# Kernel tuning notes

Measured on AMD Instinct MI355X. Metric: run time of the kernel, lower is better.

The kernel has to match this reference:

```python
import jax, jax.numpy as jnp
import numpy as np

N = 100000     # graph nodes (users + items)
NNZ = 3200000  # edges, avg degree 32
D = 128        # latent_dim
H = 64         # latent_dim // 2


def setup_inputs() -> dict:
    key = jax.random.key(0)
    ks = jax.random.split(key, 6)
    x = jax.random.normal(ks[0], (N, D), jnp.float32)
    rows = jax.random.randint(ks[1], (NNZ,), 0, N, jnp.int32)
    cols = jax.random.randint(ks[2], (NNZ,), 0, N, jnp.int32)
    # positive values ~ normalized adjacency weights
    vals = jax.random.uniform(ks[3], (NNZ,), jnp.float32) / 32.0
    # torch Linear convention: weight [out, in], xavier-uniform init, bias 0.01
    W1 = jax.random.normal(ks[4], (H, D), jnp.float32) * (6.0 / (D + H)) ** 0.5
    b1 = jnp.full((H,), 0.01, jnp.float32)
    W2 = jax.random.normal(ks[5], (1, H), jnp.float32) * (6.0 / (H + 1)) ** 0.5
    b2 = jnp.full((1,), 0.01, jnp.float32)
    t = jnp.zeros((1,), jnp.float32)  # ODE time, unused by the math
    return dict(t=t, x=x, rows=rows, cols=cols, vals=vals, W1=W1, b1=b1, W2=W2, b2=b2)


def _spmm(rows, cols, vals, x):
    # sparse (COO) @ dense: out[r] += vals[e] * x[cols[e]] for edges e with rows[e]==r
    return jax.ops.segment_sum(vals[:, None] * x[cols], rows, num_segments=x.shape[0])


def reference(t, x, rows, cols, vals, W1, b1, W2, b2):
    # gate: sigmoid(Linear(clamp(Linear(x))))  -> [N, 1]
    hidden = jnp.clip(x @ W1.T + b1, -10.0, 10.0)
    alph = jax.nn.sigmoid(hidden @ W2.T + b2)
    alph = jnp.clip(alph, 1e-6, 1.0 - 1e-6)
    # two-hop graph diffusion: alph * (A @ (A @ x)) - x
    ax = _spmm(rows, cols, vals, x)
    ax = alph * _spmm(rows, cols, vals, ax)
    return ax - x
```

## Files before the change

### kernel.cpp

```cpp
#include <hip/hip_runtime.h>
#include <stdint.h>

typedef unsigned int uint;
typedef unsigned short ushort;
typedef float f32x2 __attribute__((ext_vector_type(2)));
typedef float f32x4v __attribute__((ext_vector_type(4)));
typedef short short8 __attribute__((ext_vector_type(8)));

#define NBC_MAX 512
#define VAL7_SCALE 4064.0f
#define VAL7_INV   (1.0f / 4064.0f)
#define CUR_STRIDE 16

__device__ __forceinline__ ushort f2bf(float f) {
    uint u = __float_as_uint(f);
    return (ushort)((u + 0x7fffu + ((u >> 16) & 1u)) >> 16);
}


__global__ __launch_bounds__(256) void k_bhist(const int* __restrict__ rows,
                                               uint* __restrict__ bhist, int nnz, int nb) {
    __shared__ uint h[NBC_MAX];
    for (int j = threadIdx.x; j < nb; j += blockDim.x) h[j] = 0;
    __syncthreads();
    int stride = gridDim.x * blockDim.x;
    for (int i = blockIdx.x * blockDim.x + threadIdx.x; i < nnz; i += stride)
        atomicAdd(&h[rows[i] >> 8], 1u);
    __syncthreads();
    for (int j = threadIdx.x; j < nb; j += blockDim.x) {
        uint c = h[j];
        if (c) atomicAdd(&bhist[j], c);
    }
}


__global__ __launch_bounds__(256) void k_scan(const uint* __restrict__ bhist,
                                              uint* __restrict__ off, uint* __restrict__ cur,
                                              uint* __restrict__ row_off,
                                              int nb, int nnz, int N) {
    __shared__ uint wsum[4];
    __shared__ uint carry;
    int t = threadIdx.x, lane = t & 63, wv = t >> 6;
    if (t == 0) carry = 0;
    __syncthreads();
    for (int base = 0; base < nb; base += 256) {
        int i = base + t;
        uint v = (i < nb) ? bhist[i] : 0u;
        uint inc = v;
#pragma unroll
        for (int o = 1; o < 64; o <<= 1) { uint u = __shfl_up(inc, o); if (lane >= o) inc += u; }
        if (lane == 63) wsum[wv] = inc;
        __syncthreads();
        uint woff = 0;
        for (int k = 0; k < wv; k++) woff += wsum[k];
        uint excl = carry + woff + (inc - v);
        if (i < nb) { off[i] = excl; cur[i * CUR_STRIDE] = excl; }
        uint tot = wsum[0] + wsum[1] + wsum[2] + wsum[3];
        __syncthreads();
        if (t == 0) carry += tot;
        __syncthreads();
    }
    if (t == 0) { off[nb] = (uint)nnz; row_off[N] = (uint)nnz; }
}


__global__ __launch_bounds__(512) void k_binpass(const int* __restrict__ rows,
                                                 const int* __restrict__ cols,
                                                 const float* __restrict__ vals,
                                                 uint* __restrict__ cur, uint* __restrict__ stage,
                                                 int nnz, int nb) {
    __shared__ uint lh[NBC_MAX];
    __shared__ uint gb[NBC_MAX];
    long long beg = ((long long)blockIdx.x * nnz) / gridDim.x;
    long long end = ((long long)(blockIdx.x + 1) * nnz) / gridDim.x;
    for (int j = threadIdx.x; j < nb; j += blockDim.x) lh[j] = 0;
    __syncthreads();
    {
        long long i = beg + threadIdx.x;
        for (; i + 1536 < end; i += 2048) {
            int r0 = __builtin_nontemporal_load(rows + i);
            int r1 = __builtin_nontemporal_load(rows + i + 512);
            int r2 = __builtin_nontemporal_load(rows + i + 1024);
            int r3 = __builtin_nontemporal_load(rows + i + 1536);
            atomicAdd(&lh[r0 >> 8], 1u);
            atomicAdd(&lh[r1 >> 8], 1u);
            atomicAdd(&lh[r2 >> 8], 1u);
            atomicAdd(&lh[r3 >> 8], 1u);
        }
        for (; i < end; i += 512)
            atomicAdd(&lh[__builtin_nontemporal_load(rows + i) >> 8], 1u);
    }
    __syncthreads();
    for (int j = threadIdx.x; j < nb; j += blockDim.x) {
        uint c = lh[j];
        gb[j] = c ? atomicAdd(&cur[j * CUR_STRIDE], c) : 0u;
        lh[j] = 0;
    }
    __syncthreads();
    {
        long long i = beg + threadIdx.x;
        for (; i + 1536 < end; i += 2048) {
            int r0 = __builtin_nontemporal_load(rows + i);
            int r1 = __builtin_nontemporal_load(rows + i + 512);
            int r2 = __builtin_nontemporal_load(rows + i + 1024);
            int r3 = __builtin_nontemporal_load(rows + i + 1536);
            uint c0 = (uint)__builtin_nontemporal_load(cols + i);
            uint c1 = (uint)__builtin_nontemporal_load(cols + i + 512);
            uint c2 = (uint)__builtin_nontemporal_load(cols + i + 1024);
            uint c3 = (uint)__builtin_nontemporal_load(cols + i + 1536);
            float v0 = __builtin_nontemporal_load(vals + i);
            float v1 = __builtin_nontemporal_load(vals + i + 512);
            float v2 = __builtin_nontemporal_load(vals + i + 1024);
            float v3 = __builtin_nontemporal_load(vals + i + 1536);
            uint p0 = gb[r0 >> 8] + atomicAdd(&lh[r0 >> 8], 1u);
            uint p1 = gb[r1 >> 8] + atomicAdd(&lh[r1 >> 8], 1u);
            uint p2 = gb[r2 >> 8] + atomicAdd(&lh[r2 >> 8], 1u);
            uint p3 = gb[r3 >> 8] + atomicAdd(&lh[r3 >> 8], 1u);
            uint q0 = (uint)fminf(v0 * VAL7_SCALE + 0.5f, 127.f);
            uint q1 = (uint)fminf(v1 * VAL7_SCALE + 0.5f, 127.f);
            uint q2 = (uint)fminf(v2 * VAL7_SCALE + 0.5f, 127.f);
            uint q3 = (uint)fminf(v3 * VAL7_SCALE + 0.5f, 127.f);
            stage[p0] = ((uint)(r0 & 255) << 24) | (c0 << 7) | q0;
            stage[p1] = ((uint)(r1 & 255) << 24) | (c1 << 7) | q1;
            stage[p2] = ((uint)(r2 & 255) << 24) | (c2 << 7) | q2;
            stage[p3] = ((uint)(r3 & 255) << 24) | (c3 << 7) | q3;
        }
        for (; i < end; i += 512) {
            int r = __builtin_nontemporal_load(rows + i);
            int b = r >> 8;
            uint pos = gb[b] + atomicAdd(&lh[b], 1u);
            uint c = (uint)__builtin_nontemporal_load(cols + i);
            float v = __builtin_nontemporal_load(vals + i);
            uint q = (uint)fminf(v * VAL7_SCALE + 0.5f, 127.f);
            stage[pos] = ((uint)(r & 255) << 24) | (c << 7) | q;
        }
    }
}


__global__ __launch_bounds__(1024) void k_bsort(const uint* __restrict__ boff,
                                                const uint* __restrict__ stage,
                                                uint* __restrict__ sorted,
                                                uint* __restrict__ row_off,
                                                int N) {
    __shared__ uint rcnt[256], rcur[256];
    __shared__ uint wsum[4];
    int b = blockIdx.x;
    uint s = boff[b], e = boff[b + 1];
    int t = threadIdx.x;
    if (t < 256) rcnt[t] = 0;
    __syncthreads();
    for (uint i = s + t; i < e; i += blockDim.x)
        atomicAdd(&rcnt[stage[i] >> 24], 1u);
    __syncthreads();
    int lane = t & 63, wv = t >> 6;
    uint v = 0, inc = 0;
    if (t < 256) {
        v = rcnt[t];
        inc = v;
#pragma unroll
        for (int o = 1; o < 64; o <<= 1) { uint u = __shfl_up(inc, o); if (lane >= o) inc += u; }
        if (lane == 63) wsum[wv] = inc;
    }
    __syncthreads();
    if (t < 256) {
        uint woff = 0;
        for (int k = 0; k < wv; k++) woff += wsum[k];
        uint excl = woff + inc - v;
        rcur[t] = excl;
        int r = (b << 8) + t;
        if (r < N) row_off[r] = s + excl;
    }
    __syncthreads();
    for (uint i = s + t; i < e; i += blockDim.x) {
        uint rec = stage[i];
        uint pos = atomicAdd(&rcur[rec >> 24], 1u);
        sorted[s + pos] = rec & 0x00FFFFFFu;
    }
}


__global__ __launch_bounds__(256) void k_gatemfma(const float* __restrict__ x,
                                                  const float* __restrict__ W1,
                                                  const float* __restrict__ b1,
                                                  const float* __restrict__ W2,
                                                  const float* __restrict__ b2,
                                                  float* __restrict__ alph,
                                                  unsigned char* __restrict__ xf8, int N) {
    int lane = threadIdx.x & 63;
    int gw = (blockIdx.x * blockDim.x + threadIdx.x) >> 6;
    int nwaves = (gridDim.x * blockDim.x) >> 6;
    int g = lane >> 4;
    int r16 = lane & 15;

    short8 Bfrag[4][4];
#pragma unroll
    for (int c = 0; c < 4; c++) {
        const float* wrow = W1 + (size_t)(c * 16 + r16) * 128 + g * 8;
#pragma unroll
        for (int t = 0; t < 4; t++) {
            float4 f0 = *(const float4*)(wrow + t * 32);
            float4 f1 = *(const float4*)(wrow + t * 32 + 4);
            short8 s;
            s[0] = (short)f2bf(f0.x); s[1] = (short)f2bf(f0.y);
            s[2] = (short)f2bf(f0.z); s[3] = (short)f2bf(f0.w);
            s[4] = (short)f2bf(f1.x); s[5] = (short)f2bf(f1.y);
            s[6] = (short)f2bf(f1.z); s[7] = (short)f2bf(f1.w);
            Bfrag[c][t] = s;
        }
    }
    float b1c[4], w2c[4];
#pragma unroll
    for (int c = 0; c < 4; c++) { b1c[c] = b1[c * 16 + r16]; w2c[c] = W2[c * 16 + r16]; }
    float b2s = b2[0];

    int ntiles = (N + 15) >> 4;
    for (int tile = gw; tile < ntiles; tile += nwaves) {
        int n0 = tile << 4;
        int nrow = n0 + r16;
        int nclamp = nrow < N ? nrow : N - 1;
        const float* xrow = x + ((size_t)nclamp << 7) + g * 8;
        f32x4v acc0 = {0.f, 0.f, 0.f, 0.f}, acc1 = {0.f, 0.f, 0.f, 0.f};
        f32x4v acc2 = {0.f, 0.f, 0.f, 0.f}, acc3 = {0.f, 0.f, 0.f, 0.f};
#pragma unroll
        for (int t = 0; t < 4; t++) {
            float4 f0 = *(const float4*)(xrow + t * 32);
            float4 f1 = *(const float4*)(xrow + t * 32 + 4);
            if (nrow < N) {
                int pk0 = __builtin_amdgcn_cvt_pk_fp8_f32(f0.x, f0.y, 0, false);
                pk0 = __builtin_amdgcn_cvt_pk_fp8_f32(f0.z, f0.w, pk0, true);
                int pk1 = __builtin_amdgcn_cvt_pk_fp8_f32(f1.x, f1.y, 0, false);
                pk1 = __builtin_amdgcn_cvt_pk_fp8_f32(f1.z, f1.w, pk1, true);
                uint* xb = (uint*)(xf8 + ((size_t)nrow << 7) + t * 32 + g * 8);
                xb[0] = (uint)pk0;
                xb[1] = (uint)pk1;
            }
            short8 A;
            A[0] = (short)f2bf(f0.x); A[1] = (short)f2bf(f0.y);
            A[2] = (short)f2bf(f0.z); A[3] = (short)f2bf(f0.w);
            A[4] = (short)f2bf(f1.x); A[5] = (short)f2bf(f1.y);
            A[6] = (short)f2bf(f1.z); A[7] = (short)f2bf(f1.w);
            acc0 = __builtin_amdgcn_mfma_f32_16x16x32_bf16(A, Bfrag[0][t], acc0, 0, 0, 0);
            acc1 = __builtin_amdgcn_mfma_f32_16x16x32_bf16(A, Bfrag[1][t], acc1, 0, 0, 0);
            acc2 = __builtin_amdgcn_mfma_f32_16x16x32_bf16(A, Bfrag[2][t], acc2, 0, 0, 0);
            acc3 = __builtin_amdgcn_mfma_f32_16x16x32_bf16(A, Bfrag[3][t], acc3, 0, 0, 0);
        }
        float pr0 = 0.f, pr1 = 0.f, pr2 = 0.f, pr3 = 0.f;
#pragma unroll
        for (int r = 0; r < 4; r++) {
            float h0 = fminf(fmaxf(acc0[r] + b1c[0], -10.f), 10.f) * w2c[0];
            float h1 = fminf(fmaxf(acc1[r] + b1c[1], -10.f), 10.f) * w2c[1];
            float h2 = fminf(fmaxf(acc2[r] + b1c[2], -10.f), 10.f) * w2c[2];
            float h3 = fminf(fmaxf(acc3[r] + b1c[3], -10.f), 10.f) * w2c[3];
            float s = (h0 + h1) + (h2 + h3);
            if (r == 0) pr0 = s; else if (r == 1) pr1 = s;
            else if (r == 2) pr2 = s; else pr3 = s;
        }
#pragma unroll
        for (int o = 1; o < 16; o <<= 1) {
            pr0 += __shfl_xor(pr0, o);
            pr1 += __shfl_xor(pr1, o);
            pr2 += __shfl_xor(pr2, o);
            pr3 += __shfl_xor(pr3, o);
        }
        if (r16 < 4) {
            float p = r16 == 0 ? pr0 : r16 == 1 ? pr1 : r16 == 2 ? pr2 : pr3;
            float a = 1.f / (1.f + __expf(-(p + b2s)));
            a = fminf(fmaxf(a, 1e-6f), 1.f - 1e-6f);
            int node = n0 + g * 4 + r16;
            if (node < N) alph[node] = a;
        }
    }
}


__global__ __launch_bounds__(256) void k_spmm1(const uint* __restrict__ roff,
                                               const uint* __restrict__ recs,
                                               const unsigned char* __restrict__ xf8,
                                               unsigned char* __restrict__ axf8, int N) {
    int w = (blockIdx.x * blockDim.x + threadIdx.x) >> 6;
    int lane = threadIdx.x & 63;
    if (w >= N) return;
    uint beg = (uint)__builtin_amdgcn_readfirstlane(roff[w]);
    uint end = (uint)__builtin_amdgcn_readfirstlane(roff[w + 1]);
    float s0[8], s1[8];
#pragma unroll
    for (int k = 0; k < 8; k++) { s0[k] = 0.f; s1[k] = 0.f; }
    uint e = beg;
    for (; e + 8 <= end; e += 8) {
#pragma unroll
        for (int k = 0; k < 8; k++) {
            uint q = __builtin_nontemporal_load(recs + e + k);
            ushort u = *(const ushort*)(xf8 + ((size_t)(q >> 7) << 7) + (lane << 1));
            float v = (float)(q & 0x7Fu) * VAL7_INV;
            f32x2 f = __builtin_amdgcn_cvt_pk_f32_fp8((int)u, false);
            s0[k] = fmaf(v, f.x, s0[k]);
            s1[k] = fmaf(v, f.y, s1[k]);
        }
    }
    for (; e < end; e++) {
        uint q = __builtin_nontemporal_load(recs + e);
        ushort u = *(const ushort*)(xf8 + ((size_t)(q >> 7) << 7) + (lane << 1));
        float v = (float)(q & 0x7Fu) * VAL7_INV;
        f32x2 f = __builtin_amdgcn_cvt_pk_f32_fp8((int)u, false);
        s0[0] = fmaf(v, f.x, s0[0]);
        s1[0] = fmaf(v, f.y, s1[0]);
    }
    float a0 = ((s0[0] + s0[1]) + (s0[2] + s0[3])) + ((s0[4] + s0[5]) + (s0[6] + s0[7]));
    float a1 = ((s1[0] + s1[1]) + (s1[2] + s1[3])) + ((s1[4] + s1[5]) + (s1[6] + s1[7]));
    int pk = __builtin_amdgcn_cvt_pk_fp8_f32(a0, a1, 0, false);
    *(ushort*)(axf8 + ((size_t)w << 7) + (lane << 1)) = (ushort)(pk & 0xffff);
}


__global__ __launch_bounds__(256) void k_spmm2(const uint* __restrict__ roff,
                                               const uint* __restrict__ recs,
                                               const unsigned char* __restrict__ axf8,
                                               const float* __restrict__ alph,
                                               const float* __restrict__ x,
                                               float* __restrict__ out, int N) {
    int w = (blockIdx.x * blockDim.x + threadIdx.x) >> 6;
    int lane = threadIdx.x & 63;
    if (w >= N) return;
    uint beg = (uint)__builtin_amdgcn_readfirstlane(roff[w]);
    uint end = (uint)__builtin_amdgcn_readfirstlane(roff[w + 1]);
    float s0[8], s1[8];
#pragma unroll
    for (int k = 0; k < 8; k++) { s0[k] = 0.f; s1[k] = 0.f; }
    uint e = beg;
    for (; e + 8 <= end; e += 8) {
#pragma unroll
        for (int k = 0; k < 8; k++) {
            uint q = __builtin_nontemporal_load(recs + e + k);
            ushort u = *(const ushort*)(axf8 + ((size_t)(q >> 7) << 7) + (lane << 1));
            float v = (float)(q & 0x7Fu) * VAL7_INV;
            f32x2 f = __builtin_amdgcn_cvt_pk_f32_fp8((int)u, false);
            s0[k] = fmaf(v, f.x, s0[k]);
            s1[k] = fmaf(v, f.y, s1[k]);
        }
    }
    for (; e < end; e++) {
        uint q = __builtin_nontemporal_load(recs + e);
        ushort u = *(const ushort*)(axf8 + ((size_t)(q >> 7) << 7) + (lane << 1));
        float v = (float)(q & 0x7Fu) * VAL7_INV;
        f32x2 f = __builtin_amdgcn_cvt_pk_f32_fp8((int)u, false);
        s0[0] = fmaf(v, f.x, s0[0]);
        s1[0] = fmaf(v, f.y, s1[0]);
    }
    float a0 = ((s0[0] + s0[1]) + (s0[2] + s0[3])) + ((s0[4] + s0[5]) + (s0[6] + s0[7]));
    float a1 = ((s1[0] + s1[1]) + (s1[2] + s1[3])) + ((s1[4] + s1[5]) + (s1[6] + s1[7]));
    float al = alph[w];
    const f32x2* xp = (const f32x2*)(x + ((size_t)w << 7)) + lane;
    f32x2 xr = __builtin_nontemporal_load(xp);
    f32x2 o;
    o.x = fmaf(al, a0, -xr.x);
    o.y = fmaf(al, a1, -xr.y);
    __builtin_nontemporal_store(o, (f32x2*)out + ((size_t)w << 6) + lane);
}


extern "C" void kernel_launch(void* const* d_in, const int* in_sizes, int n_in,
                              void* d_out, int out_size, void* d_ws, size_t ws_size,
                              hipStream_t stream) {
    const float* x    = (const float*)d_in[1];
    const int*   rows = (const int*)d_in[2];
    const int*   cols = (const int*)d_in[3];
    const float* vals = (const float*)d_in[4];
    const float* W1 = (const float*)d_in[5];
    const float* b1 = (const float*)d_in[6];
    const float* W2 = (const float*)d_in[7];
    const float* b2 = (const float*)d_in[8];
    float* out = (float*)d_out;

    int N = in_sizes[1] / 128;
    int nnz = in_sizes[2];
    int nb = (N + 255) >> 8;

    char* ws = (char*)d_ws;
    size_t off_b = 0;
    auto take = [&](size_t bytes) -> char* {
        size_t p = (off_b + 255) & ~(size_t)255;
        off_b = p + bytes;
        return ws + p;
    };
    uint*   stage  = (uint*)take((size_t)nnz * 4);
    unsigned char* xf8 = (unsigned char*)take((size_t)N * 128);
    uint*   sorted = (uint*)take((size_t)nnz * 4);
    unsigned char* axf8 = (unsigned char*)take((size_t)N * 128);
    float*  alph   = (float*)take((size_t)N * 4);
    uint*   bhist  = (uint*)take((size_t)(nb + 1) * 4);
    uint*   boff   = (uint*)take((size_t)(nb + 1) * 4);
    uint*   bcur   = (uint*)take((size_t)(nb + 1) * 4 * CUR_STRIDE);
    uint*   row_off = (uint*)take((size_t)(N + 1) * 4);
    (void)ws_size; (void)n_in; (void)out_size;

    hipMemsetAsync(bhist, 0, (size_t)nb * 4, stream);
    k_bhist<<<120, 256, 0, stream>>>(rows, bhist, nnz, nb);
    k_scan<<<1, 256, 0, stream>>>(bhist, boff, bcur, row_off, nb, nnz, N);
    k_binpass<<<1024, 512, 0, stream>>>(rows, cols, vals, bcur, stage, nnz, nb);
    k_bsort<<<nb, 1024, 0, stream>>>(boff, stage, sorted, row_off, N);
    k_gatemfma<<<512, 256, 0, stream>>>(x, W1, b1, W2, b2, alph, xf8, N);
    k_spmm1<<<((N * 64) + 255) / 256, 256, 0, stream>>>(row_off, sorted, xf8, axf8, N);
    k_spmm2<<<((N * 64) + 255) / 256, 256, 0, stream>>>(row_off, sorted, axf8, alph, x, out, N);
}
```

Measured before the change: 296.6 us.

## Replace atomic bin cursor with per-block count matrix and two-level scan

The bucket sort pre-pass previously built a global histogram, scanned it, then had each binning block reserve space with global atomics on bin cursors, reading the rows array three times. It now writes per-block bin counts to a matrix, scans each bin column across blocks, and scans the bin totals, so the scatter kernel gets deterministic offsets without global atomics. This removes the separate histogram pass and the cursor contention, at the cost of a 1024×nb count matrix and two extra small kernel launches. The k_cscan kernel hardcodes 16 counts per lane across 64 lanes, which ties it to NBLK=1024.

New measurement: 251.7 us. -15.1%, faster.

```diff
diff --git a/kernel.cpp b/kernel.cpp
--- a/kernel.cpp
+++ b/kernel.cpp
@@ -8,9 +8,9 @@
 typedef short short8 __attribute__((ext_vector_type(8)));
 
 #define NBC_MAX 512
+#define NBLK 1024
 #define VAL7_SCALE 4064.0f
 #define VAL7_INV   (1.0f / 4064.0f)
-#define CUR_STRIDE 16
 
 __device__ __forceinline__ ushort f2bf(float f) {
     uint u = __float_as_uint(f);
@@ -18,59 +18,9 @@
 }
 
 
-__global__ __launch_bounds__(256) void k_bhist(const int* __restrict__ rows,
-                                               uint* __restrict__ bhist, int nnz, int nb) {
-    __shared__ uint h[NBC_MAX];
-    for (int j = threadIdx.x; j < nb; j += blockDim.x) h[j] = 0;
-    __syncthreads();
-    int stride = gridDim.x * blockDim.x;
-    for (int i = blockIdx.x * blockDim.x + threadIdx.x; i < nnz; i += stride)
-        atomicAdd(&h[rows[i] >> 8], 1u);
-    __syncthreads();
-    for (int j = threadIdx.x; j < nb; j += blockDim.x) {
-        uint c = h[j];
-        if (c) atomicAdd(&bhist[j], c);
-    }
-}
-
-
-__global__ __launch_bounds__(256) void k_scan(const uint* __restrict__ bhist,
-                                              uint* __restrict__ off, uint* __restrict__ cur,
-                                              uint* __restrict__ row_off,
-                                              int nb, int nnz, int N) {
-    __shared__ uint wsum[4];
-    __shared__ uint carry;
-    int t = threadIdx.x, lane = t & 63, wv = t >> 6;
-    if (t == 0) carry = 0;
-    __syncthreads();
-    for (int base = 0; base < nb; base += 256) {
-        int i = base + t;
-        uint v = (i < nb) ? bhist[i] : 0u;
-        uint inc = v;
-#pragma unroll
-        for (int o = 1; o < 64; o <<= 1) { uint u = __shfl_up(inc, o); if (lane >= o) inc += u; }
-        if (lane == 63) wsum[wv] = inc;
-        __syncthreads();
-        uint woff = 0;
-        for (int k = 0; k < wv; k++) woff += wsum[k];
-        uint excl = carry + woff + (inc - v);
-        if (i < nb) { off[i] = excl; cur[i * CUR_STRIDE] = excl; }
-        uint tot = wsum[0] + wsum[1] + wsum[2] + wsum[3];
-        __syncthreads();
-        if (t == 0) carry += tot;
-        __syncthreads();
-    }
-    if (t == 0) { off[nb] = (uint)nnz; row_off[N] = (uint)nnz; }
-}
-
-
-__global__ __launch_bounds__(512) void k_binpass(const int* __restrict__ rows,
-                                                 const int* __restrict__ cols,
-                                                 const float* __restrict__ vals,
-                                                 uint* __restrict__ cur, uint* __restrict__ stage,
-                                                 int nnz, int nb) {
+__global__ __launch_bounds__(512) void k_count(const int* __restrict__ rows,
+                                               uint* __restrict__ C, int nnz, int nb) {
     __shared__ uint lh[NBC_MAX];
-    __shared__ uint gb[NBC_MAX];
     long long beg = ((long long)blockIdx.x * nnz) / gridDim.x;
     long long end = ((long long)(blockIdx.x + 1) * nnz) / gridDim.x;
     for (int j = threadIdx.x; j < nb; j += blockDim.x) lh[j] = 0;
@@ -91,10 +41,81 @@
             atomicAdd(&lh[__builtin_nontemporal_load(rows + i) >> 8], 1u);
     }
     __syncthreads();
+    for (int j = threadIdx.x; j < nb; j += blockDim.x)
+        C[(size_t)blockIdx.x * nb + j] = lh[j];
+}
+
+
+__global__ __launch_bounds__(256) void k_cscan(uint* __restrict__ C,
+                                               uint* __restrict__ T, int nb) {
+    int wv = (blockIdx.x * blockDim.x + threadIdx.x) >> 6;
+    int lane = threadIdx.x & 63;
+    if (wv >= nb) return;
+    uint v[16];
+    uint s = 0;
+#pragma unroll
+    for (int k = 0; k < 16; k++) {
+        v[k] = C[(size_t)(lane * 16 + k) * nb + wv];
+        s += v[k];
+    }
+    uint inc = s;
+#pragma unroll
+    for (int o = 1; o < 64; o <<= 1) { uint u = __shfl_up(inc, o); if (lane >= o) inc += u; }
+    uint run = inc - s;
+#pragma unroll
+    for (int k = 0; k < 16; k++) {
+        uint t = v[k];
+        C[(size_t)(lane * 16 + k) * nb + wv] = run;
+        run += t;
+    }
+    if (lane == 63) T[wv] = inc;
+}
+
+
+__global__ __launch_bounds__(256) void k_scan(const uint* __restrict__ T,
+                                              uint* __restrict__ off,
+                                              uint* __restrict__ row_off,
+                                              int nb, int nnz, int N) {
+    __shared__ uint wsum[4];
+    __shared__ uint carry;
+    int t = threadIdx.x, lane = t & 63, wv = t >> 6;
+    if (t == 0) carry = 0;
+    __syncthreads();
+    for (int base = 0; base < nb; base += 256) {
+        int i = base + t;
+        uint v = (i < nb) ? T[i] : 0u;
+        uint inc = v;
+#pragma unroll
+        for (int o = 1; o < 64; o <<= 1) { uint u = __shfl_up(inc, o); if (lane >= o) inc += u; }
+        if (lane == 63) wsum[wv] = inc;
+        __syncthreads();
+        uint woff = 0;
+        for (int k = 0; k < wv; k++) woff += wsum[k];
+        uint excl = carry + woff + (inc - v);
+        if (i < nb) off[i] = excl;
+        uint tot = wsum[0] + wsum[1] + wsum[2] + wsum[3];
+        __syncthreads();
+        if (t == 0) carry += tot;
+        __syncthreads();
+    }
+    if (t == 0) { off[nb] = (uint)nnz; row_off[N] = (uint)nnz; }
+}
+
+
+__global__ __launch_bounds__(512) void k_scatter(const int* __restrict__ rows,
+                                                 const int* __restrict__ cols,
+                                                 const float* __restrict__ vals,
+                                                 const uint* __restrict__ C,
+                                                 const uint* __restrict__ boff,
+                                                 uint* __restrict__ stage,
+                                                 int nnz, int nb) {
+    __shared__ uint lh[NBC_MAX];
+    __shared__ uint gb[NBC_MAX];
+    long long beg = ((long long)blockIdx.x * nnz) / gridDim.x;
+    long long end = ((long long)(blockIdx.x + 1) * nnz) / gridDim.x;
     for (int j = threadIdx.x; j < nb; j += blockDim.x) {
-        uint c = lh[j];
-        gb[j] = c ? atomicAdd(&cur[j * CUR_STRIDE], c) : 0u;
         lh[j] = 0;
+        gb[j] = boff[j] + C[(size_t)blockIdx.x * nb + j];
     }
     __syncthreads();
     {
@@ -388,16 +409,18 @@
     uint*   sorted = (uint*)take((size_t)nnz * 4);
     unsigned char* axf8 = (unsigned char*)take((size_t)N * 128);
     float*  alph   = (float*)take((size_t)N * 4);
-    uint*   bhist  = (uint*)take((size_t)(nb + 1) * 4);
+    uint*   C      = (uint*)take((size_t)NBLK * nb * 4);
+    uint*   T      = (uint*)take((size_t)(nb + 1) * 4);
     uint*   boff   = (uint*)take((size_t)(nb + 1) * 4);
-    uint*   bcur   = (uint*)take((size_t)(nb + 1) * 4 * CUR_STRIDE);
     uint*   row_off = (uint*)take((size_t)(N + 1) * 4);
     (void)ws_size; (void)n_in; (void)out_size;
 
-    hipMemsetAsync(bhist, 0, (size_t)nb * 4, stream);
-    k_bhist<<<120, 256, 0, stream>>>(rows, bhist, nnz, nb);
-    k_scan<<<1, 256, 0, stream>>>(bhist, boff, bcur, row_off, nb, nnz, N);
-    k_binpass<<<1024, 512, 0, stream>>>(rows, cols, vals, bcur, stage, nnz, nb);
+    int cscan_blocks = (nb * 64 + 255) / 256;
+
+    k_count<<<NBLK, 512, 0, stream>>>(rows, C, nnz, nb);
+    k_cscan<<<cscan_blocks, 256, 0, stream>>>(C, T, nb);
+    k_scan<<<1, 256, 0, stream>>>(T, boff, row_off, nb, nnz, N);
+    k_scatter<<<NBLK, 512, 0, stream>>>(rows, cols, vals, C, boff, stage, nnz, nb);
     k_bsort<<<nb, 1024, 0, stream>>>(boff, stage, sorted, row_off, N);
     k_gatemfma<<<512, 256, 0, stream>>>(x, W1, b1, W2, b2, alph, xf8, N);
     k_spmm1<<<((N * 64) + 255) / 256, 256, 0, stream>>>(row_off, sorted, xf8, axf8, N);
```
